# Optimization experiments

Measured on AMD Instinct MI355X. Metric: run time of the kernel, lower is better.

The kernel has to match this reference:

```python
import jax, jax.numpy as jnp
import numpy as np
from jax import lax

L, B, F = 1024, 2, 1024
E = 2
H = E * F          # ssm_features = 2048
N = 16             # state_dim
R = F // N         # dt_rank = 64
K = 4              # conv kernel size
DT_MIN, DT_MAX = 0.001, 0.1


def setup_inputs() -> dict:
    key = jax.random.key(0)
    ks = jax.random.split(key, 6)
    def w(k, shape, fan_in):
        return jax.random.normal(k, shape, jnp.float32) / np.float32(np.sqrt(fan_in))
    x = jax.random.normal(ks[0], (L, B, F), jnp.float32)
    W_in = w(ks[1], (F, 2 * H), F)
    W_conv = w(ks[2], (K, H // E, H), K * (H // E))  # flax Conv kernel (K, in/groups, out), groups=E
    b_conv = jnp.zeros((H,), jnp.float32)
    A_log = jnp.log(jnp.broadcast_to(jnp.arange(1, N + 1, dtype=jnp.float32), (H, N)))
    D = jnp.ones((H,), jnp.float32)
    W_ssm = w(ks[3], (H, R + 2 * N), H)
    W_dt = w(ks[4], (R, H), R)
    b_dt = jnp.zeros((H,), jnp.float32)
    W_out = w(ks[5], (H, F), H)
    return dict(x=x, W_in=W_in, W_conv=W_conv, b_conv=b_conv, A_log=A_log, D=D,
                W_ssm=W_ssm, W_dt=W_dt, b_dt=b_dt, W_out=W_out)


def _selective_scan(u, dt, A, Bm, Cm, D):
    # u, dt: (L,B,H); A: (H,N); Bm, Cm: (L,B,N); D: (H,)
    dt = jnp.clip(dt, DT_MIN, DT_MAX)
    dA = jnp.exp(jnp.einsum('lbh,hn->lbhn', dt, A))          # (L,B,H,N)
    dBu = jnp.einsum('lbh,lbn->lbhn', dt * u, Bm)            # (L,B,H,N)
    def comb(s, c):
        return (c[0] * s[0], c[0] * s[1] + c[1])
    _, xs = lax.associative_scan(comb, (dA, dBu), axis=0)
    y = jnp.einsum('lbn,lbhn->lbh', Cm, xs)
    return y + u * D


def reference(x, W_in, W_conv, b_conv, A_log, D, W_ssm, W_dt, b_dt, W_out):
    # in_proj (no bias) then split into ssm branch and gate residual
    h = x @ W_in                                             # (L,B,2H)
    xs, res = jnp.split(h, 2, axis=-1)                       # each (L,B,H)
    # causal grouped conv over time: rearrange (L,B,H)->(B,L,H), NWC layout
    xc = jnp.transpose(xs, (1, 0, 2))
    xc = lax.conv_general_dilated(
        xc, W_conv, window_strides=(1,), padding=[(K - 1, 0)],
        dimension_numbers=('NWC', 'WIO', 'NWC'), feature_group_count=E) + b_conv
    xs = jnp.transpose(xc, (1, 0, 2))                        # (L,B,H)
    u = jax.nn.silu(xs)
    # SSM
    A = -jnp.exp(A_log)                                      # (H,N)
    proj = u @ W_ssm                                         # (L,B,N+N+R)
    Bm = proj[..., :N]
    Cm = proj[..., N:2 * N]
    dt = proj[..., 2 * N:]
    delta = jax.nn.softplus(dt @ W_dt + b_dt)                # (L,B,H)
    y = _selective_scan(u, delta, A, Bm, Cm, D)
    # gate and out_proj (no bias)
    return (y * jax.nn.silu(res)) @ W_out                    # (L,B,F)
```

## Files before the change

kernel.cpp:

```cpp
#include <hip/hip_runtime.h>
#include <math.h>


typedef unsigned short u16;
typedef unsigned int u32;
typedef __attribute__((ext_vector_type(8))) short short8;
typedef __attribute__((ext_vector_type(4))) float floatx4;
typedef __attribute__((ext_vector_type(4))) u16 ushort4v;

__device__ __forceinline__ u16 f2bf(float f) {
    u32 u = __float_as_uint(f);
    return (u16)((u + 0x7fffu + ((u >> 16) & 1u)) >> 16);
}
__device__ __forceinline__ float bf2f(u16 v) {
    return __uint_as_float((u32)v << 16);
}
__device__ __forceinline__ float fexp2(float x) {
    return __builtin_amdgcn_exp2f(x);
}

__device__ __forceinline__ float dpp_red16(float v) {
    v += __uint_as_float((u32)__builtin_amdgcn_update_dpp(
        0, (int)__float_as_uint(v), 0xB1, 0xF, 0xF, true));
    v += __uint_as_float((u32)__builtin_amdgcn_update_dpp(
        0, (int)__float_as_uint(v), 0x4E, 0xF, 0xF, true));
    v += __uint_as_float((u32)__builtin_amdgcn_update_dpp(
        0, (int)__float_as_uint(v), 0x141, 0xF, 0xF, true));
    v += __uint_as_float((u32)__builtin_amdgcn_update_dpp(
        0, (int)__float_as_uint(v), 0x128, 0xF, 0xF, true));
    return v;
}

__device__ __forceinline__ void gl_lds16(const u16* g, u16* l) {
    auto gp = reinterpret_cast<const __attribute__((address_space(1))) u32*>(
        reinterpret_cast<uintptr_t>(g));
    auto lp = reinterpret_cast<__attribute__((address_space(3))) u32*>(
        reinterpret_cast<uintptr_t>(l));
    __builtin_amdgcn_global_load_lds(gp, lp, 16, 0, 0);
}

__device__ __forceinline__ void trans_dev(const float* __restrict__ S,
                                          u16* __restrict__ D, int R, int C,
                                          int bx, int by)
{
    __shared__ u16 t[64][65];
    int br = bx * 64;
    int bc = by * 64;
    int c = threadIdx.x & 63;
    int r0 = threadIdx.x >> 6;
#pragma unroll
    for (int i = 0; i < 16; ++i) {
        int r = r0 + i * 4;
        float v = 0.f;
        if (br + r < R && bc + c < C) v = S[(size_t)(br + r) * C + bc + c];
        t[r][c] = f2bf(v);
    }
    __syncthreads();
    int cc0 = threadIdx.x >> 4;
    int rr0 = (threadIdx.x & 15) * 4;
#pragma unroll
    for (int i = 0; i < 4; ++i) {
        int cc = i * 16 + cc0;
        if (bc + cc < C) {
            ushort4v o;
#pragma unroll
            for (int k = 0; k < 4; ++k) o[k] = t[rr0 + k][cc];
            *(ushort4v*)(D + (size_t)(bc + cc) * R + br + rr0) = o;
        }
    }
}

__global__ __launch_bounds__(256) void prep_k(
    const float* __restrict__ Wc, u16* __restrict__ WTc,
    const float* __restrict__ Wi, u16* __restrict__ WTi,
    const float* __restrict__ Wo, u16* __restrict__ WTo,
    const float* __restrict__ Ws, u16* __restrict__ WTs,
    const float* __restrict__ Wd, u16* __restrict__ WTd,
    const float* __restrict__ x,  u16* __restrict__ xb)
{
    int b = blockIdx.x;
    if (b < 2048) { trans_dev(Wc, WTc, 4096, 2048, b & 63, b >> 6); return; }
    b -= 2048;
    if (b < 1024) { trans_dev(Wi, WTi, 1024, 4096, b & 15, b >> 4); return; }
    b -= 1024;
    if (b < 512)  { trans_dev(Wo, WTo, 2048, 1024, b & 31, b >> 5); return; }
    b -= 512;
    if (b < 64)   { trans_dev(Ws, WTs, 2048, 96,   b & 31, b >> 5); return; }
    b -= 64;
    if (b < 32)   { trans_dev(Wd, WTd, 64, 2048,   0,      b);      return; }
    b -= 32;
    {
        int i = (b * 256 + threadIdx.x) * 4;
        float4 v = *(const float4*)(x + i);
        u16 o[4] = {f2bf(v.x), f2bf(v.y), f2bf(v.z), f2bf(v.w)};
        *(ulong1*)(xb + i) = *(ulong1*)o;
    }
}

__global__ __launch_bounds__(256) void tbf_k(const u16* __restrict__ S,
                                             u16* __restrict__ D)
{
    __shared__ u16 t[64][68];
    int br = blockIdx.x * 64;
    int bc = blockIdx.y * 64;
    int c = threadIdx.x & 63;
    int r0 = threadIdx.x >> 6;
#pragma unroll
    for (int i = 0; i < 16; ++i) {
        int r = r0 + i * 4;
        t[r][c] = S[(size_t)(br + r) * 2048 + bc + c];
    }
    __syncthreads();
#pragma unroll
    for (int i = 0; i < 16; ++i) {
        int r = r0 + i * 4;
        D[(size_t)(bc + r) * 2048 + br + c] = t[c][r];
    }
}

__global__ __launch_bounds__(256) void cvtp_k(const float* __restrict__ proj,
                                              u16* __restrict__ pb,
                                              u16* __restrict__ bc)
{
    if (blockIdx.x < 128) {
        int g = blockIdx.x * 256 + threadIdx.x;
        int m = g >> 4, i = (g & 15) * 4;
        float4 v = *(const float4*)(proj + (size_t)m * 128 + 64 + i);
        u16 o[4] = {f2bf(v.x), f2bf(v.y), f2bf(v.z), f2bf(v.w)};
        *(ulong1*)(pb + (size_t)m * 64 + i) = *(ulong1*)o;
    } else {
        int g = (blockIdx.x - 128) * 256 + threadIdx.x;
        int m = g >> 3, i = (g & 7) * 4;
        float4 v = *(const float4*)(proj + (size_t)m * 128 + i);
        u16 o[4] = {f2bf(v.x), f2bf(v.y), f2bf(v.z), f2bf(v.w)};
        *(ulong1*)(bc + (size_t)m * 32 + i) = *(ulong1*)o;
    }
}

template<int MODE>
__global__ __launch_bounds__(256) void gls_k(
    const u16* __restrict__ A, int lda,
    const u16* __restrict__ B, int ldb,
    float* __restrict__ Cf, int ldc,
    u16* __restrict__ Cb0, u16* __restrict__ Cb1,
    const float* __restrict__ bias, int nkt)
{
    __shared__ u16 As[128 * 64];
    __shared__ u16 Bs[64 * 64];
    const int tid = threadIdx.x;
    const int bm = blockIdx.y * 128;
    const int bn = blockIdx.x * 64;
    const int kofs = (MODE == 3) ? blockIdx.z * nkt * 64 : 0;
    const int lane = tid & 63, wave = tid >> 6, wm = wave * 32;
    const int m16 = lane & 15, q = lane >> 4;
    floatx4 acc[2][4] = {};

    const int rsub = lane >> 3;
    const int pch  = lane & 7;

    for (int kt = 0; kt < nkt; ++kt) {
        const int k0 = kofs + kt * 64;
#pragma unroll
        for (int i = 0; i < 4; ++i) {
            int r = i * 32 + wave * 8 + rsub;
            int c = pch ^ (r & 7);
            gl_lds16(A + (size_t)(bm + r) * lda + k0 + c * 8,
                     As + i * 2048 + wave * 512);
        }
#pragma unroll
        for (int i = 0; i < 2; ++i) {
            int r = i * 32 + wave * 8 + rsub;
            int c = pch ^ (r & 7);
            gl_lds16(B + (size_t)(bn + r) * ldb + k0 + c * 8,
                     Bs + i * 2048 + wave * 512);
        }
        __syncthreads();

#pragma unroll
        for (int ks = 0; ks < 2; ++ks) {
            short8 af[2], bfr[4];
#pragma unroll
            for (int ti = 0; ti < 2; ++ti) {
                int r = wm + ti * 16 + m16;
                int p = (ks * 4 + q) ^ (r & 7);
                af[ti] = *(const short8*)(As + r * 64 + p * 8);
            }
#pragma unroll
            for (int tj = 0; tj < 4; ++tj) {
                int r = tj * 16 + m16;
                int p = (ks * 4 + q) ^ (r & 7);
                bfr[tj] = *(const short8*)(Bs + r * 64 + p * 8);
            }
#pragma unroll
            for (int ti = 0; ti < 2; ++ti)
#pragma unroll
                for (int tj = 0; tj < 4; ++tj)
                    acc[ti][tj] = __builtin_amdgcn_mfma_f32_16x16x32_bf16(
                        af[ti], bfr[tj], acc[ti][tj], 0, 0, 0);
        }
        __syncthreads();
    }

    if (MODE == 3) {
#pragma unroll
        for (int tj = 0; tj < 4; ++tj) {
            int gn = bn + tj * 16 + m16;
#pragma unroll
            for (int ti = 0; ti < 2; ++ti) {
                int gm0 = bm + wm + ti * 16 + q * 4;
#pragma unroll
                for (int r = 0; r < 4; ++r)
                    atomicAdd(Cf + (size_t)(gm0 + r) * ldc + gn, acc[ti][tj][r]);
            }
        }
        return;
    }
    if (MODE == 0 && bn >= 2048) {
#pragma unroll
        for (int tj = 0; tj < 4; ++tj) {
            int gn = bn + tj * 16 + m16;
#pragma unroll
            for (int ti = 0; ti < 2; ++ti) {
                int gm0 = bm + wm + ti * 16 + q * 4;
                ushort4v h;
#pragma unroll
                for (int r = 0; r < 4; ++r) h[r] = f2bf(acc[ti][tj][r]);
                *(ushort4v*)(Cb1 + (size_t)(gn - 2048) * 2048 + gm0) = h;
            }
        }
        return;
    }
#pragma unroll
    for (int tj = 0; tj < 4; ++tj) {
#pragma unroll
        for (int ti = 0; ti < 2; ++ti) {
            int lr0 = wm + ti * 16 + q * 4;
#pragma unroll
            for (int r = 0; r < 4; ++r)
                As[(lr0 + r) * 64 + tj * 16 + m16] = f2bf(acc[ti][tj][r]);
        }
    }
    __syncthreads();
    {
        int row = tid >> 1, half = tid & 1;
        u16* gdst = Cb0 + (size_t)(bm + row) * 2048 + bn + half * 32;
        const u16* lsrc = As + row * 64 + half * 32;
#pragma unroll
        for (int i = 0; i < 4; ++i)
            *(short8*)(gdst + i * 8) = *(const short8*)(lsrc + i * 8);
    }
}

__global__ __launch_bounds__(256) void conv2_k(
    const u16* __restrict__ A,
    const u16* __restrict__ B,
    const float* __restrict__ bias,
    u16* __restrict__ Cb0,
    u16* __restrict__ Cb1)
{
    __shared__ u16 Astrip[136 * 64];
    __shared__ u16 Bs[4 * 64 * 64];
    const int tid = threadIdx.x;
    const int bm = blockIdx.y * 128;
    const int bn = blockIdx.x * 64;
    const int gofs = (bn >= 1024) ? 1024 : 0;
    const int lane = tid & 63, wave = tid >> 6, wm = wave * 32;
    const int m16 = lane & 15, q = lane >> 4;
    floatx4 acc[2][4] = {};
    const int rsub = lane >> 3;
    const int pch  = lane & 7;

    for (int ch = 0; ch < 16; ++ch) {
        const int ck = ch * 64;
#pragma unroll
        for (int i = 0; i < 4; ++i) {
            int r = i * 32 + wave * 8 + rsub;
            int c = pch ^ (r & 7);
            int rg = bm + r - 6;
            if (rg < 0) rg = 0;
            gl_lds16(A + (size_t)rg * 2048 + gofs + ck + c * 8,
                     Astrip + i * 2048 + wave * 512);
        }
        if (wave == 0) {
            int r = 128 + rsub;
            int c = pch ^ (r & 7);
            int rg = bm + r - 6;
            if (rg > 2047) rg = 2047;
            gl_lds16(A + (size_t)rg * 2048 + gofs + ck + c * 8,
                     Astrip + 4 * 2048);
        }
#pragma unroll
        for (int t = 0; t < 4; ++t)
#pragma unroll
            for (int i = 0; i < 2; ++i) {
                int r = i * 32 + wave * 8 + rsub;
                int c = pch ^ (r & 7);
                gl_lds16(B + (size_t)(bn + r) * 4096 + t * 1024 + ck + c * 8,
                         Bs + t * 4096 + i * 2048 + wave * 512);
            }
        if (bm == 0) {
            asm volatile("s_waitcnt vmcnt(0)" ::: "memory");
            if (tid < 48)
                *(short8*)(Astrip + (tid >> 3) * 64 + (tid & 7) * 8) = short8{};
        }
        __syncthreads();

#pragma unroll
        for (int t = 0; t < 4; ++t) {
#pragma unroll
            for (int ks = 0; ks < 2; ++ks) {
                short8 af[2], bfr[4];
#pragma unroll
                for (int ti = 0; ti < 2; ++ti) {
                    int sr = wm + ti * 16 + m16 + 2 * t;
                    int p = (ks * 4 + q) ^ (sr & 7);
                    af[ti] = *(const short8*)(Astrip + sr * 64 + p * 8);
                }
#pragma unroll
                for (int tj = 0; tj < 4; ++tj) {
                    int br = tj * 16 + m16;
                    int p = (ks * 4 + q) ^ (br & 7);
                    bfr[tj] = *(const short8*)(Bs + t * 4096 + br * 64 + p * 8);
                }
#pragma unroll
                for (int ti = 0; ti < 2; ++ti)
#pragma unroll
                    for (int tj = 0; tj < 4; ++tj)
                        acc[ti][tj] = __builtin_amdgcn_mfma_f32_16x16x32_bf16(
                            af[ti], bfr[tj], acc[ti][tj], 0, 0, 0);
            }
        }
        __syncthreads();
    }

#pragma unroll
    for (int tj = 0; tj < 4; ++tj) {
        int gn = bn + tj * 16 + m16;
        float bv = bias[gn];
#pragma unroll
        for (int ti = 0; ti < 2; ++ti) {
            int lr0 = wm + ti * 16 + q * 4;
            ushort4v h;
#pragma unroll
            for (int r = 0; r < 4; ++r) {
                float v = acc[ti][tj][r] + bv;
                v = v / (1.f + __expf(-v));
                u16 hv = f2bf(v);
                h[r] = hv;
                Astrip[(lr0 + r) * 64 + tj * 16 + m16] = hv;
            }
            *(ushort4v*)(Cb1 + (size_t)gn * 2048 + bm + lr0) = h;
        }
    }
    __syncthreads();
    {
        int row = tid >> 1, half = tid & 1;
        u16* gdst = Cb0 + (size_t)(bm + row) * 2048 + bn + half * 32;
        const u16* lsrc = Astrip + row * 64 + half * 32;
#pragma unroll
        for (int i = 0; i < 4; ++i)
            *(short8*)(gdst + i * 8) = *(const short8*)(lsrc + i * 8);
    }
}

#define APAD 40
__global__ __launch_bounds__(256) void g3_k(
    const u16* __restrict__ A,
    const u16* __restrict__ Bw,
    float* __restrict__ proj)
{
    __shared__ u16 As[128 * APAD];
    __shared__ u16 Bs[64 * APAD];
    const int tid = threadIdx.x;
    const int bn = blockIdx.x * 64;
    const int bm = blockIdx.y * 128;
    const int kb = blockIdx.z * 256;
    const int lane = tid & 63, wave = tid >> 6, wm = wave * 32;
    const int m16 = lane & 15, q = lane >> 4;
    floatx4 acc[2][4] = {};
    const int ar = tid >> 2, ac = (tid & 3) * 8;

    for (int kt = 0; kt < 8; ++kt) {
        const int k0 = kb + kt * 32;
#pragma unroll
        for (int p = 0; p < 2; ++p) {
            int r = ar + p * 64;
            *(short8*)(As + r * APAD + ac) =
                *(const short8*)(A + (size_t)(bm + r) * 2048 + k0 + ac);
        }
        *(short8*)(Bs + ar * APAD + ac) =
            *(const short8*)(Bw + (size_t)(bn + ar) * 2048 + k0 + ac);
        __syncthreads();

        short8 af[2], bfr[4];
#pragma unroll
        for (int ti = 0; ti < 2; ++ti)
            af[ti] = *(const short8*)(As + (wm + ti * 16 + m16) * APAD + q * 8);
#pragma unroll
        for (int tj = 0; tj < 4; ++tj)
            bfr[tj] = *(const short8*)(Bs + (tj * 16 + m16) * APAD + q * 8);
#pragma unroll
        for (int ti = 0; ti < 2; ++ti)
#pragma unroll
            for (int tj = 0; tj < 4; ++tj)
                acc[ti][tj] = __builtin_amdgcn_mfma_f32_16x16x32_bf16(
                    af[ti], bfr[tj], acc[ti][tj], 0, 0, 0);
        __syncthreads();
    }

#pragma unroll
    for (int tj = 0; tj < 4; ++tj) {
        int gn = bn + tj * 16 + m16;
        if (gn >= 96) continue;
        int col = (gn < 16) ? (2 * gn) : (gn < 32 ? 2 * (gn - 16) + 1 : 32 + gn);
#pragma unroll
        for (int ti = 0; ti < 2; ++ti)
#pragma unroll
            for (int r = 0; r < 4; ++r) {
                int gm = bm + wm + ti * 16 + q * 4 + r;
                atomicAdd(proj + (size_t)gm * 128 + col, acc[ti][tj][r]);
            }
    }
}

__global__ __launch_bounds__(256) void g4_k(
    const u16* __restrict__ A,
    const u16* __restrict__ B,
    const float* __restrict__ bias,
    float* __restrict__ Cf)
{
    __shared__ u16 As[128 * APAD];
    __shared__ u16 Bs[64 * APAD];
    const int tid = threadIdx.x;
    const int bm = blockIdx.y * 128;
    const int bn = blockIdx.x * 64;
    const int lane = tid & 63, wave = tid >> 6, wm = wave * 32;
    const int m16 = lane & 15, q = lane >> 4;
    floatx4 acc[2][4] = {};
    const int ar = tid >> 2, ac = (tid & 3) * 8;

    for (int kt = 0; kt < 2; ++kt) {
        const int k0 = kt * 32;
#pragma unroll
        for (int p = 0; p < 2; ++p) {
            int r = ar + p * 64;
            *(short8*)(As + r * APAD + ac) =
                *(const short8*)(A + (size_t)(bm + r) * 64 + k0 + ac);
        }
        *(short8*)(Bs + ar * APAD + ac) =
            *(const short8*)(B + (size_t)(bn + ar) * 64 + k0 + ac);
        __syncthreads();
        short8 af[2], bfr[4];
#pragma unroll
        for (int ti = 0; ti < 2; ++ti)
            af[ti] = *(const short8*)(As + (wm + ti * 16 + m16) * APAD + q * 8);
#pragma unroll
        for (int tj = 0; tj < 4; ++tj)
            bfr[tj] = *(const short8*)(Bs + (tj * 16 + m16) * APAD + q * 8);
#pragma unroll
        for (int ti = 0; ti < 2; ++ti)
#pragma unroll
            for (int tj = 0; tj < 4; ++tj)
                acc[ti][tj] = __builtin_amdgcn_mfma_f32_16x16x32_bf16(
                    af[ti], bfr[tj], acc[ti][tj], 0, 0, 0);
        __syncthreads();
    }
#pragma unroll
    for (int tj = 0; tj < 4; ++tj) {
        int gn = bn + tj * 16 + m16;
        float bv = bias[gn];
#pragma unroll
        for (int ti = 0; ti < 2; ++ti) {
            int gm0 = bm + wm + ti * 16 + q * 4;
            float t[4];
#pragma unroll
            for (int r = 0; r < 4; ++r) {
                float v = acc[ti][tj][r] + bv;
                v = (v > 15.f) ? v : log1pf(__expf(v));
                t[r] = fminf(fmaxf(v, 0.001f), 0.1f);
            }
            *(float4*)(Cf + (size_t)gn * 2048 + gm0) =
                make_float4(t[0], t[1], t[2], t[3]);
        }
    }
}

__global__ __launch_bounds__(512) void scan7_k(
    const float* __restrict__ deltaT,
    const u16* __restrict__ uT,
    const u16* __restrict__ bc16,
    const float* __restrict__ A_log,
    const float* __restrict__ Dvec,
    const u16* __restrict__ resT,
    u16* __restrict__ zT)
{
    __shared__ float lP[2][32][16], lS[2][32][16], lI[2][32][16];
    __shared__ float yrow[2048];
    const int h = blockIdx.x;
    const int tid = threadIdx.x;
    const int n = tid & 15;
    const int c = tid >> 4;
    const int l0 = c * 32;

    const float An2 = -__expf(A_log[h * 16 + n]) * 1.442695041f;
    const float* drow = deltaT + (size_t)h * 2048;
    const u16*   urow = uT     + (size_t)h * 2048;

    float s0 = 0.f, s1 = 0.f, T0 = 0.f, T1 = 0.f;
    for (int j = 0; j < 32; ++j) {
        int l = l0 + j;
        float2 dtv = *(const float2*)(drow + 2 * l);
        u32 uv = *(const u32*)(urow + 2 * l);
        float uu0 = __uint_as_float(uv << 16);
        float uu1 = __uint_as_float(uv & 0xffff0000u);
        u32 w0 = *(const u32*)(bc16 + (size_t)(2 * l) * 32 + 2 * n);
        u32 w1 = *(const u32*)(bc16 + (size_t)(2 * l + 1) * 32 + 2 * n);
        float e0 = fexp2(dtv.x * An2);
        float e1 = fexp2(dtv.y * An2);
        s0 = fmaf(e0, s0, dtv.x * uu0 * __uint_as_float(w0 << 16));
        s1 = fmaf(e1, s1, dtv.y * uu1 * __uint_as_float(w1 << 16));
        T0 += dtv.x;
        T1 += dtv.y;
    }
    lP[0][c][n] = fexp2(T0 * An2); lS[0][c][n] = s0;
    lP[1][c][n] = fexp2(T1 * An2); lS[1][c][n] = s1;
    __syncthreads();
    if (tid < 32) {
        int bb = tid >> 4, nn = tid & 15;
        float X = 0.f;
#pragma unroll
        for (int cc = 0; cc < 32; ++cc) {
            lI[bb][cc][nn] = X;
            X = fmaf(lP[bb][cc][nn], X, lS[bb][cc][nn]);
        }
    }
    __syncthreads();

    s0 = lI[0][c][n];
    s1 = lI[1][c][n];
    const float Dh = Dvec[h];
    for (int j = 0; j < 32; ++j) {
        int l = l0 + j;
        float2 dtv = *(const float2*)(drow + 2 * l);
        u32 uv = *(const u32*)(urow + 2 * l);
        float uu0 = __uint_as_float(uv << 16);
        float uu1 = __uint_as_float(uv & 0xffff0000u);
        u32 w0 = *(const u32*)(bc16 + (size_t)(2 * l) * 32 + 2 * n);
        u32 w1 = *(const u32*)(bc16 + (size_t)(2 * l + 1) * 32 + 2 * n);
        float e0 = fexp2(dtv.x * An2);
        float e1 = fexp2(dtv.y * An2);
        s0 = fmaf(e0, s0, dtv.x * uu0 * __uint_as_float(w0 << 16));
        s1 = fmaf(e1, s1, dtv.y * uu1 * __uint_as_float(w1 << 16));
        float v0 = dpp_red16(__uint_as_float(w0 & 0xffff0000u) * s0);
        float v1 = dpp_red16(__uint_as_float(w1 & 0xffff0000u) * s1);
        if (n == 0) {
            yrow[2 * l]     = v0 + uu0 * Dh;
            yrow[2 * l + 1] = v1 + uu1 * Dh;
        }
    }
    __syncthreads();
    {
        int t0 = tid * 4;
        ushort4v rv = *(const ushort4v*)(resT + (size_t)h * 2048 + t0);
        u16 o[4];
#pragma unroll
        for (int i = 0; i < 4; ++i) {
            float r = bf2f(rv[i]);
            float y = yrow[t0 + i];
            o[i] = f2bf(y * (r / (1.f + __expf(-r))));
        }
        *(ulong1*)(zT + (size_t)h * 2048 + t0) = *(ulong1*)o;
    }
}

extern "C" void kernel_launch(void* const* d_in, const int* in_sizes, int n_in,
                              void* d_out, int out_size, void* d_ws, size_t ws_size,
                              hipStream_t stream)
{
    const float* x      = (const float*)d_in[0];
    const float* W_in   = (const float*)d_in[1];
    const float* W_conv = (const float*)d_in[2];
    const float* b_conv = (const float*)d_in[3];
    const float* A_log  = (const float*)d_in[4];
    const float* Dv     = (const float*)d_in[5];
    const float* W_ssm  = (const float*)d_in[6];
    const float* W_dt   = (const float*)d_in[7];
    const float* b_dt   = (const float*)d_in[8];
    const float* W_out  = (const float*)d_in[9];
    float* out = (float*)d_out;

    char* wsc = (char*)d_ws;
    u16*   xb     = (u16*)wsc;
    float* projb  = (float*)wsc;
    u16*   pb_dt  = (u16*)(wsc + (2u << 20));
    u16*   bc16   = (u16*)(wsc + (3u << 20));
    u16*   WT_in  = (u16*)(wsc + (4u << 20));
    u16*   u_mh   = (u16*)(wsc + (4u << 20));
    u16*   z_mh   = (u16*)(wsc + (4u << 20));
    u16*   xsbf   = (u16*)(wsc + (12u << 20));
    u16*   zT     = xsbf;
    u16*   resT   = (u16*)(wsc + (20u << 20));
    u16*   WT_cv  = (u16*)(wsc + (28u << 20));
    float* deltaT = (float*)(wsc + (28u << 20));
    u16*   uT     = (u16*)(wsc + (44u << 20));
    u16*   WT_out = (u16*)(wsc + (52u << 20));
    u16*   WT_ssm = (u16*)(wsc + (56u << 20));
    u16*   WT_dt  = (u16*)(wsc + (56u << 20) + (512u << 10));

    dim3 blk(256);

    prep_k<<<dim3(5728), blk, 0, stream>>>(
        W_conv, WT_cv, W_in, WT_in, W_out, WT_out, W_ssm, WT_ssm, W_dt, WT_dt,
        x, xb);

    hipMemsetAsync(out, 0, 2048 * 1024 * sizeof(float), stream);

    gls_k<0><<<dim3(64, 16), blk, 0, stream>>>(
        xb, 1024, WT_in, 1024, nullptr, 0, xsbf, resT, nullptr, 16);

    hipMemsetAsync(projb, 0, 2048 * 128 * sizeof(float), stream);

    conv2_k<<<dim3(32, 16), blk, 0, stream>>>(xsbf, WT_cv, b_conv, u_mh, uT);

    g3_k<<<dim3(2, 16, 8), blk, 0, stream>>>(u_mh, WT_ssm, projb);

    cvtp_k<<<dim3(192), blk, 0, stream>>>(projb, pb_dt, bc16);

    g4_k<<<dim3(32, 16), blk, 0, stream>>>(pb_dt, WT_dt, b_dt, deltaT);

    scan7_k<<<dim3(2048), dim3(512), 0, stream>>>(
        deltaT, uT, bc16, A_log, Dv, resT, zT);

    tbf_k<<<dim3(32, 32), blk, 0, stream>>>(zT, z_mh);

    gls_k<3><<<dim3(16, 16, 2), blk, 0, stream>>>(
        z_mh, 2048, WT_out, 2048, out, 1024, nullptr, nullptr, nullptr, 16);
}
```

Measured before the change: 317.8 us.

## Enlarge GEMM tiles to 128x128 and fold memsets and dt conversion into kernels

The GEMM kernel now uses 128x128 output tiles, with each wave owning a 64x64 sub-tile, to get more operand reuse per LDS load. The out-projection now splits K four ways instead of two, which means more atomic adds. The two memsets are folded into existing kernels: output zeroing moves into prep_k and proj zeroing into conv2_k. The dt-branch fp32-to-bf16 conversion is fused into g4_k's load path, so cvtp_k now converts only the B/C columns. Together these remove launches and an intermediate buffer, at the cost of higher register and LDS pressure, fewer blocks for the in-projection, and more atomic contention.

```diff
diff --git a/kernel.cpp b/kernel.cpp
--- a/kernel.cpp
+++ b/kernel.cpp
@@ -76,7 +76,8 @@
     const float* __restrict__ Wo, u16* __restrict__ WTo,
     const float* __restrict__ Ws, u16* __restrict__ WTs,
     const float* __restrict__ Wd, u16* __restrict__ WTd,
-    const float* __restrict__ x,  u16* __restrict__ xb)
+    const float* __restrict__ x,  u16* __restrict__ xb,
+    float* __restrict__ outz)
 {
     int b = blockIdx.x;
     if (b < 2048) { trans_dev(Wc, WTc, 4096, 2048, b & 63, b >> 6); return; }
@@ -89,11 +90,17 @@
     b -= 64;
     if (b < 32)   { trans_dev(Wd, WTd, 64, 2048,   0,      b);      return; }
     b -= 32;
-    {
+    if (b < 2048) {
         int i = (b * 256 + threadIdx.x) * 4;
         float4 v = *(const float4*)(x + i);
         u16 o[4] = {f2bf(v.x), f2bf(v.y), f2bf(v.z), f2bf(v.w)};
         *(ulong1*)(xb + i) = *(ulong1*)o;
+        return;
+    }
+    b -= 2048;
+    {
+        int i = (b * 256 + threadIdx.x) * 4;
+        *(float4*)(outz + i) = make_float4(0.f, 0.f, 0.f, 0.f);
     }
 }
 
@@ -119,44 +126,34 @@
 }
 
 __global__ __launch_bounds__(256) void cvtp_k(const float* __restrict__ proj,
-                                              u16* __restrict__ pb,
                                               u16* __restrict__ bc)
 {
-    if (blockIdx.x < 128) {
-        int g = blockIdx.x * 256 + threadIdx.x;
-        int m = g >> 4, i = (g & 15) * 4;
-        float4 v = *(const float4*)(proj + (size_t)m * 128 + 64 + i);
-        u16 o[4] = {f2bf(v.x), f2bf(v.y), f2bf(v.z), f2bf(v.w)};
-        *(ulong1*)(pb + (size_t)m * 64 + i) = *(ulong1*)o;
-    } else {
-        int g = (blockIdx.x - 128) * 256 + threadIdx.x;
-        int m = g >> 3, i = (g & 7) * 4;
-        float4 v = *(const float4*)(proj + (size_t)m * 128 + i);
-        u16 o[4] = {f2bf(v.x), f2bf(v.y), f2bf(v.z), f2bf(v.w)};
-        *(ulong1*)(bc + (size_t)m * 32 + i) = *(ulong1*)o;
-    }
+    int g = blockIdx.x * 256 + threadIdx.x;
+    int m = g >> 3, i = (g & 7) * 4;
+    float4 v = *(const float4*)(proj + (size_t)m * 128 + i);
+    u16 o[4] = {f2bf(v.x), f2bf(v.y), f2bf(v.z), f2bf(v.w)};
+    *(ulong1*)(bc + (size_t)m * 32 + i) = *(ulong1*)o;
 }
 
 template<int MODE>
-__global__ __launch_bounds__(256) void gls_k(
+__global__ __launch_bounds__(256) void gls2_k(
     const u16* __restrict__ A, int lda,
     const u16* __restrict__ B, int ldb,
     float* __restrict__ Cf, int ldc,
-    u16* __restrict__ Cb0, u16* __restrict__ Cb1,
-    const float* __restrict__ bias, int nkt)
-{
-    __shared__ u16 As[128 * 64];
-    __shared__ u16 Bs[64 * 64];
+    u16* __restrict__ Cb0, u16* __restrict__ Cb1, int nkt)
+{
+    __shared__ u16 S[128 * 128];
+    u16* As = S;
+    u16* Bs = S + 8192;
     const int tid = threadIdx.x;
     const int bm = blockIdx.y * 128;
-    const int bn = blockIdx.x * 64;
+    const int bn = blockIdx.x * 128;
     const int kofs = (MODE == 3) ? blockIdx.z * nkt * 64 : 0;
-    const int lane = tid & 63, wave = tid >> 6, wm = wave * 32;
+    const int lane = tid & 63, wave = tid >> 6;
+    const int wm = (wave & 1) * 64, wn = (wave >> 1) * 64;
     const int m16 = lane & 15, q = lane >> 4;
-    floatx4 acc[2][4] = {};
-
-    const int rsub = lane >> 3;
-    const int pch  = lane & 7;
+    floatx4 acc[4][4] = {};
+    const int rsub = lane >> 3, pch = lane & 7;
 
     for (int kt = 0; kt < nkt; ++kt) {
         const int k0 = kofs + kt * 64;
@@ -166,11 +163,6 @@
             int c = pch ^ (r & 7);
             gl_lds16(A + (size_t)(bm + r) * lda + k0 + c * 8,
                      As + i * 2048 + wave * 512);
-        }
-#pragma unroll
-        for (int i = 0; i < 2; ++i) {
-            int r = i * 32 + wave * 8 + rsub;
-            int c = pch ^ (r & 7);
             gl_lds16(B + (size_t)(bn + r) * ldb + k0 + c * 8,
                      Bs + i * 2048 + wave * 512);
         }
@@ -178,21 +170,21 @@
 
 #pragma unroll
         for (int ks = 0; ks < 2; ++ks) {
-            short8 af[2], bfr[4];
-#pragma unroll
-            for (int ti = 0; ti < 2; ++ti) {
+            short8 af[4], bfr[4];
+#pragma unroll
+            for (int ti = 0; ti < 4; ++ti) {
                 int r = wm + ti * 16 + m16;
                 int p = (ks * 4 + q) ^ (r & 7);
                 af[ti] = *(const short8*)(As + r * 64 + p * 8);
             }
 #pragma unroll
             for (int tj = 0; tj < 4; ++tj) {
-                int r = tj * 16 + m16;
+                int r = wn + tj * 16 + m16;
                 int p = (ks * 4 + q) ^ (r & 7);
                 bfr[tj] = *(const short8*)(Bs + r * 64 + p * 8);
             }
 #pragma unroll
-            for (int ti = 0; ti < 2; ++ti)
+            for (int ti = 0; ti < 4; ++ti)
 #pragma unroll
                 for (int tj = 0; tj < 4; ++tj)
                     acc[ti][tj] = __builtin_amdgcn_mfma_f32_16x16x32_bf16(
@@ -204,9 +196,9 @@
     if (MODE == 3) {
 #pragma unroll
         for (int tj = 0; tj < 4; ++tj) {
-            int gn = bn + tj * 16 + m16;
-#pragma unroll
-            for (int ti = 0; ti < 2; ++ti) {
+            int gn = bn + wn + tj * 16 + m16;
+#pragma unroll
+            for (int ti = 0; ti < 4; ++ti) {
                 int gm0 = bm + wm + ti * 16 + q * 4;
 #pragma unroll
                 for (int r = 0; r < 4; ++r)
@@ -215,38 +207,39 @@
         }
         return;
     }
-    if (MODE == 0 && bn >= 2048) {
+    if (bn >= 2048) {
 #pragma unroll
         for (int tj = 0; tj < 4; ++tj) {
-            int gn = bn + tj * 16 + m16;
-#pragma unroll
-            for (int ti = 0; ti < 2; ++ti) {
+            int gn = bn - 2048 + wn + tj * 16 + m16;
+#pragma unroll
+            for (int ti = 0; ti < 4; ++ti) {
                 int gm0 = bm + wm + ti * 16 + q * 4;
                 ushort4v h;
 #pragma unroll
                 for (int r = 0; r < 4; ++r) h[r] = f2bf(acc[ti][tj][r]);
-                *(ushort4v*)(Cb1 + (size_t)(gn - 2048) * 2048 + gm0) = h;
+                *(ushort4v*)(Cb1 + (size_t)gn * 2048 + gm0) = h;
             }
         }
         return;
     }
 #pragma unroll
     for (int tj = 0; tj < 4; ++tj) {
-#pragma unroll
-        for (int ti = 0; ti < 2; ++ti) {
+        int col = wn + tj * 16 + m16;
+#pragma unroll
+        for (int ti = 0; ti < 4; ++ti) {
             int lr0 = wm + ti * 16 + q * 4;
 #pragma unroll
             for (int r = 0; r < 4; ++r)
-                As[(lr0 + r) * 64 + tj * 16 + m16] = f2bf(acc[ti][tj][r]);
+                S[(lr0 + r) * 128 + col] = f2bf(acc[ti][tj][r]);
         }
     }
     __syncthreads();
     {
         int row = tid >> 1, half = tid & 1;
-        u16* gdst = Cb0 + (size_t)(bm + row) * 2048 + bn + half * 32;
-        const u16* lsrc = As + row * 64 + half * 32;
-#pragma unroll
-        for (int i = 0; i < 4; ++i)
+        u16* gdst = Cb0 + (size_t)(bm + row) * 2048 + bn + half * 64;
+        const u16* lsrc = S + row * 128 + half * 64;
+#pragma unroll
+        for (int i = 0; i < 8; ++i)
             *(short8*)(gdst + i * 8) = *(const short8*)(lsrc + i * 8);
     }
 }
@@ -256,13 +249,18 @@
     const u16* __restrict__ B,
     const float* __restrict__ bias,
     u16* __restrict__ Cb0,
-    u16* __restrict__ Cb1)
+    u16* __restrict__ Cb1,
+    float* __restrict__ projz)
 {
     __shared__ u16 Astrip[136 * 64];
     __shared__ u16 Bs[4 * 64 * 64];
     const int tid = threadIdx.x;
     const int bm = blockIdx.y * 128;
     const int bn = blockIdx.x * 64;
+    {
+        int fb = blockIdx.y * gridDim.x + blockIdx.x;
+        *(float2*)(projz + fb * 512 + tid * 2) = make_float2(0.f, 0.f);
+    }
     const int gofs = (bn >= 1024) ? 1024 : 0;
     const int lane = tid & 63, wave = tid >> 6, wm = wave * 32;
     const int m16 = lane & 15, q = lane >> 4;
@@ -424,7 +422,7 @@
 }
 
 __global__ __launch_bounds__(256) void g4_k(
-    const u16* __restrict__ A,
+    const float* __restrict__ proj,
     const u16* __restrict__ B,
     const float* __restrict__ bias,
     float* __restrict__ Cf)
@@ -444,8 +442,13 @@
 #pragma unroll
         for (int p = 0; p < 2; ++p) {
             int r = ar + p * 64;
-            *(short8*)(As + r * APAD + ac) =
-                *(const short8*)(A + (size_t)(bm + r) * 64 + k0 + ac);
+            const float* src = proj + (size_t)(bm + r) * 128 + 64 + k0 + ac;
+            float4 v0 = *(const float4*)src;
+            float4 v1 = *(const float4*)(src + 4);
+            short8 v = {(short)f2bf(v0.x), (short)f2bf(v0.y), (short)f2bf(v0.z),
+                        (short)f2bf(v0.w), (short)f2bf(v1.x), (short)f2bf(v1.y),
+                        (short)f2bf(v1.z), (short)f2bf(v1.w)};
+            *(short8*)(As + r * APAD + ac) = v;
         }
         *(short8*)(Bs + ar * APAD + ac) =
             *(const short8*)(B + (size_t)(bn + ar) * 64 + k0 + ac);
@@ -592,7 +595,6 @@
     char* wsc = (char*)d_ws;
     u16*   xb     = (u16*)wsc;
     float* projb  = (float*)wsc;
-    u16*   pb_dt  = (u16*)(wsc + (2u << 20));
     u16*   bc16   = (u16*)(wsc + (3u << 20));
     u16*   WT_in  = (u16*)(wsc + (4u << 20));
     u16*   u_mh   = (u16*)(wsc + (4u << 20));
@@ -609,30 +611,27 @@
 
     dim3 blk(256);
 
-    prep_k<<<dim3(5728), blk, 0, stream>>>(
+    prep_k<<<dim3(7776), blk, 0, stream>>>(
         W_conv, WT_cv, W_in, WT_in, W_out, WT_out, W_ssm, WT_ssm, W_dt, WT_dt,
-        x, xb);
-
-    hipMemsetAsync(out, 0, 2048 * 1024 * sizeof(float), stream);
-
-    gls_k<0><<<dim3(64, 16), blk, 0, stream>>>(
-        xb, 1024, WT_in, 1024, nullptr, 0, xsbf, resT, nullptr, 16);
-
-    hipMemsetAsync(projb, 0, 2048 * 128 * sizeof(float), stream);
-
-    conv2_k<<<dim3(32, 16), blk, 0, stream>>>(xsbf, WT_cv, b_conv, u_mh, uT);
+        x, xb, out);
+
+    gls2_k<0><<<dim3(32, 16), blk, 0, stream>>>(
+        xb, 1024, WT_in, 1024, nullptr, 0, xsbf, resT, 16);
+
+    conv2_k<<<dim3(32, 16), blk, 0, stream>>>(
+        xsbf, WT_cv, b_conv, u_mh, uT, projb);
 
     g3_k<<<dim3(2, 16, 8), blk, 0, stream>>>(u_mh, WT_ssm, projb);
 
-    cvtp_k<<<dim3(192), blk, 0, stream>>>(projb, pb_dt, bc16);
-
-    g4_k<<<dim3(32, 16), blk, 0, stream>>>(pb_dt, WT_dt, b_dt, deltaT);
+    cvtp_k<<<dim3(64), blk, 0, stream>>>(projb, bc16);
+
+    g4_k<<<dim3(32, 16), blk, 0, stream>>>(projb, WT_dt, b_dt, deltaT);
 
     scan7_k<<<dim3(2048), dim3(512), 0, stream>>>(
         deltaT, uT, bc16, A_log, Dv, resT, zT);
 
     tbf_k<<<dim3(32, 32), blk, 0, stream>>>(zT, z_mh);
 
-    gls_k<3><<<dim3(16, 16, 2), blk, 0, stream>>>(
-        z_mh, 2048, WT_out, 2048, out, 1024, nullptr, nullptr, nullptr, 16);
-}
+    gls2_k<3><<<dim3(8, 16, 4), blk, 0, stream>>>(
+        z_mh, 2048, WT_out, 2048, out, 1024, nullptr, nullptr, 8);
+}
```

Result: slower. 328.1 us (+3.2%).
